# Optimization experiments

Measured on AMD Instinct MI355X. Metric: run time of the kernel, lower is better.

The kernel has to match this reference:

```python
import jax, jax.numpy as jnp
import numpy as np

B, L, E, H = 4, 2048, 1024, 16
D = E // H  # head_dim = 64
NEG_INF = -1e9


def _rope(x):
    # x: [B, L, H, D]; standard rotate-half RoPE over head_dim
    seq = x.shape[1]
    inv_freq = 1.0 / (10000.0 ** (jnp.arange(0, D, 2, dtype=jnp.float32) / D))  # [D/2]
    ang = jnp.arange(seq, dtype=jnp.float32)[:, None] * inv_freq               # [L, D/2]
    cos = jnp.concatenate([jnp.cos(ang), jnp.cos(ang)], axis=-1)[None, :, None, :]
    sin = jnp.concatenate([jnp.sin(ang), jnp.sin(ang)], axis=-1)[None, :, None, :]
    x1, x2 = jnp.split(x, 2, axis=-1)
    rot = jnp.concatenate([-x2, x1], axis=-1)
    return x * cos + rot * sin


def setup_inputs() -> dict:
    key = jax.random.key(0)
    ks = jax.random.split(key, 12)
    xavier = lambda k: jax.random.uniform(k, (E, E), jnp.float32,
                                          -np.sqrt(6.0 / (E + E)), np.sqrt(6.0 / (E + E)))
    return {
        "query": jax.random.normal(ks[0], (B, L, E), jnp.float32),
        "key": jax.random.normal(ks[1], (B, L, E), jnp.float32),
        "value": jax.random.normal(ks[2], (B, L, E), jnp.float32),
        "wq": xavier(ks[3]), "bq": jnp.zeros((E,), jnp.float32),
        "wk": xavier(ks[4]), "bk": jnp.zeros((E,), jnp.float32),
        "wv": xavier(ks[5]), "bv": jnp.zeros((E,), jnp.float32),
        "wo": xavier(ks[6]), "bo": jnp.zeros((E,), jnp.float32),
        "key_padding_mask": jax.random.randint(ks[7], (B, L), 0, 2).astype(bool),
    }


def reference(query, key, value, wq, bq, wk, bk, wv, bv, wo, bo, key_padding_mask):
    b, ql = query.shape[0], query.shape[1]
    sl = key.shape[1]
    q = (query @ wq.T + bq).reshape(b, ql, H, D)
    k = (key @ wk.T + bk).reshape(b, sl, H, D)
    v = (value @ wv.T + bv).reshape(b, sl, H, D)
    q = _rope(q)
    k = _rope(k)
    # causal mask (is_causal=True, attn_mask=None path) + key padding mask, additive
    causal = jnp.where(jnp.triu(jnp.ones((ql, sl), bool), k=1), NEG_INF, 0.0)  # [L, L]
    kpm = jnp.where(key_padding_mask[:, None, None, :], NEG_INF, 0.0)          # [B,1,1,S]
    mask = causal[None, None, :, :] + kpm
    scores = jnp.einsum("bqhd,bkhd->bhqk", q, k) / np.sqrt(D) + mask
    attn = jax.nn.softmax(scores, axis=-1)
    out = jnp.einsum("bhqk,bkhd->bqhd", attn, v).reshape(b, ql, E)
    return out @ wo.T + bo
```

## Files before the change

### kernel.cpp

```cpp
#include <hip/hip_runtime.h>

typedef unsigned short u16;
typedef unsigned int   u32;

using bf16x8 = __attribute__((ext_vector_type(8))) __bf16;
using f32x4  = __attribute__((ext_vector_type(4))) float;
using f32x16 = __attribute__((ext_vector_type(16))) float;

#define DEV static __device__ __forceinline__
#define GP(p) (const __attribute__((address_space(1))) void*)(p)
#define LP(p) (__attribute__((address_space(3))) void*)(p)
#define WAITB(N) asm volatile("s_waitcnt vmcnt(" N ")\n\ts_barrier" ::: "memory")

DEV u16 f2bf(float f){
  u32 u = __builtin_bit_cast(u32, f);
  u32 r = u + 0x7fffu + ((u>>16)&1u);
  return (u16)(r>>16);
}
DEV bf16x8 as_bf(uint4 v){ return __builtin_bit_cast(bf16x8, v); }
DEV u32 cvt_pk(float lo, float hi){
  u32 r;
  asm("v_cvt_pk_bf16_f32 %0, %1, %2" : "=v"(r) : "v"(lo), "v"(hi));
  return r;
}
DEV void plswap(u32 &a, u32 &b){
  auto r = __builtin_amdgcn_permlane32_swap((int)a, (int)b, false, false);
  a = (u32)r[0]; b = (u32)r[1];
}
DEV float fexp2(float x){ float r; asm("v_exp_f32 %0, %1" : "=v"(r) : "v"(x)); return r; }
DEV float max3f(float a, float b, float c){
  float r; asm("v_max3_f32 %0, %1, %2, %3" : "=v"(r) : "v"(a), "v"(b), "v"(c)); return r;
}
DEV float fractf_(float x){ float r; asm("v_fract_f32 %0, %1" : "=v"(r) : "v"(x)); return r; }
DEV float sinrev(float f){ float r; asm("v_sin_f32 %0, %1" : "=v"(r) : "v"(f)); return r; }
DEV float cosrev(float f){ float r; asm("v_cos_f32 %0, %1" : "=v"(r) : "v"(f)); return r; }

constexpr int CB = 4, CL = 2048, CE = 1024, CH = 16, CD = 64;
constexpr int CM = CB*CL;
constexpr float LOG2E  = 1.44269504088896f;
constexpr float NEGBIG = -1.44269504e9f;
constexpr float INV2PI = 0.15915494309189535f;

__global__ void detect_mask_kernel(const void* __restrict__ mask, int* __restrict__ flag){
  __shared__ int a_gt1, a_badf, a_oddnz, a_evennz;
  if (threadIdx.x==0){ a_gt1=0; a_badf=0; a_oddnz=0; a_evennz=0; }
  __syncthreads();
  const u32* w = (const u32*)mask;
  int gt1=0, badf=0, oddnz=0, evennz=0;
  for (int i=threadIdx.x; i<2048; i+=256){
    u32 v = w[i];
    if (v > 1u) gt1 = 1;
    if (v != 0u && v != 0x3f800000u) badf = 1;
    if (v != 0u){ if (i & 1) oddnz = 1; else evennz = 1; }
  }
  if (gt1) atomicOr(&a_gt1,1);
  if (badf) atomicOr(&a_badf,1);
  if (oddnz) atomicOr(&a_oddnz,1);
  if (evennz) atomicOr(&a_evennz,1);
  __syncthreads();
  if (threadIdx.x==0){
    int mode;
    if (!a_gt1)           mode = (!a_oddnz && a_evennz) ? 3 : 0;
    else if (!a_badf)     mode = 1;
    else                  mode = 2;
    flag[0] = mode;
  }
}

__global__ void convert_mask_kernel(const void* __restrict__ mask, const int* __restrict__ flag,
                                    float* __restrict__ maskf){
  int i = blockIdx.x*blockDim.x + threadIdx.x;
  if (i >= CB*CL) return;
  int mode = flag[0];
  int v;
  if      (mode==0) v = ((const int*)mask)[i] != 0;
  else if (mode==1) v = ((const float*)mask)[i] != 0.f;
  else if (mode==3) v = ((const int*)mask)[2*i] != 0;
  else              v = ((const unsigned char*)mask)[i] != 0;
  maskf[i] = v ? NEGBIG : 0.f;
}

__global__ void cast_all(const float* __restrict__ q, const float* __restrict__ k,
                         const float* __restrict__ v,
                         const float* __restrict__ wq, const float* __restrict__ wk,
                         const float* __restrict__ wv, const float* __restrict__ wo,
                         u16* __restrict__ oq, u16* __restrict__ ok, u16* __restrict__ ov,
                         u16* __restrict__ owq, u16* __restrict__ owk,
                         u16* __restrict__ owv, u16* __restrict__ owo){
  int i = blockIdx.x*blockDim.x + threadIdx.x;
  const float* in; u16* out; int j;
  if (i < 3*(1<<21)){
    int w = i >> 21; j = i & ((1<<21)-1);
    in = (w==0)?q:(w==1)?k:v; out = (w==0)?oq:(w==1)?ok:ov;
  } else {
    int r = i - 3*(1<<21);
    int w = r >> 18; j = r & ((1<<18)-1);
    in = (w==0)?wq:(w==1)?wk:(w==2)?wv:wo; out = (w==0)?owq:(w==1)?owk:(w==2)?owv:owo;
  }
  float4 a = ((const float4*)in)[j];
  ushort4 h;
  h.x = f2bf(a.x); h.y = f2bf(a.y); h.z = f2bf(a.z); h.w = f2bf(a.w);
  ((ushort4*)out)[j] = h;
}

__global__ __launch_bounds__(512) void gemm_qkv(
    const u16* __restrict__ qbf, const u16* __restrict__ kbf, const u16* __restrict__ vbf,
    const u16* __restrict__ wqb, const u16* __restrict__ wkb, const u16* __restrict__ wvb,
    const float* __restrict__ bq, const float* __restrict__ bk, const float* __restrict__ bv,
    u16* __restrict__ Qp, u16* __restrict__ Kp, u16* __restrict__ Vt, int zbase)
{
  __shared__ u16 As[3][16384];
  __shared__ u16 Bs[3][8192];
  const int z = zbase + blockIdx.y;
  const int tid=threadIdx.x, lane=tid&63, wid=tid>>6;
  const int llo=lane&15, lhi=lane>>4;
  const u16* A; const u16* Bt;
  if (z==0){ A=qbf; Bt=wqb; }
  else if (z==1){ A=kbf; Bt=wkb; }
  else { A=wvb; Bt=vbf; }
  int bid = blockIdx.x;
  int xcd = bid&7, j = bid>>3;
  int mb, nb;
  if (z<2){ mb = xcd*4 + (j>>3); nb = j&7; }
  else    { mb = j&3;  nb = xcd*8 + (j>>2); }
  const int m0 = mb*256, n0 = nb*128;
  const int wr = wid>>1, wc = wid&1;
  const int rswA = llo&7;

  auto STAGE = [&](int t, int buf){
    #pragma unroll
    for (int i=0;i<4;i++){
      int c = tid + i*512;
      int row = c>>3, ch = c&7;
      int sc = ch ^ (row&7);
      __builtin_amdgcn_global_load_lds(GP(A + (size_t)(m0+row)*CE + t*64 + sc*8),
                                       LP(&As[buf][c*8]), 16, 0, 0);
    }
    #pragma unroll
    for (int i=0;i<2;i++){
      int c = tid + i*512;
      int row = c>>3, ch = c&7;
      int sc = ch ^ (row&7);
      __builtin_amdgcn_global_load_lds(GP(Bt + (size_t)(n0+row)*CE + t*64 + sc*8),
                                       LP(&Bs[buf][c*8]), 16, 0, 0);
    }
  };

  f32x4 acc[4][4] = {};

  auto COMP = [&](int buf){
    const char* as = (const char*)As[buf];
    const char* bs = (const char*)Bs[buf];
    #pragma unroll
    for (int ks=0; ks<2; ks++){
      bf16x8 af[4], bf_[4];
      #pragma unroll
      for (int mr=0;mr<4;mr++){
        int r = wr*64+mr*16+llo;
        af[mr] = as_bf(*(const uint4*)(as + r*128 + (((ks*4+lhi)^rswA)<<4)));
      }
      #pragma unroll
      for (int nr=0;nr<4;nr++){
        int r = wc*64+nr*16+llo;
        bf_[nr] = as_bf(*(const uint4*)(bs + r*128 + (((ks*4+lhi)^rswA)<<4)));
      }
      #pragma unroll
      for (int mr=0;mr<4;mr++)
        #pragma unroll
        for (int nr=0;nr<4;nr++)
          acc[mr][nr] = __builtin_amdgcn_mfma_f32_16x16x32_bf16(af[mr], bf_[nr], acc[mr][nr], 0,0,0);
    }
  };

  STAGE(0,0); STAGE(1,1);
  WAITB("6");

  #pragma unroll 1
  for (int t=0; t<14; t++){
    STAGE(t+2, (t+2)%3);
    COMP(t%3);
    WAITB("6");
  }
  COMP(2); WAITB("0");
  COMP(0);

  const int colbase = n0 + wc*64;
  if (z < 2){
    const float* bias = z ? bk : bq;
    u16* outp = z ? Kp : Qp;
    const float scale = z ? 1.f : 0.125f*LOG2E;
    const int h = colbase >> 6;
    float b1[2], b2[2], invr[2];
    #pragma unroll
    for (int nr=0;nr<2;nr++){
      int j2 = nr*16 + llo;
      b1[nr] = bias[colbase + j2];
      b2[nr] = bias[colbase + j2 + 32];
      invr[nr] = exp2f(-(float)j2 * 0.41524101186092033f) * INV2PI;
    }
    #pragma unroll
    for (int mr=0;mr<4;mr++)
      #pragma unroll
      for (int r=0;r<4;r++){
        int row = m0 + wr*64 + mr*16 + lhi*4 + r;
        int b = row >> 11, l = row & 2047;
        u16* dst = outp + (((size_t)(b*CH + h)*CL + l) << 6);
        #pragma unroll
        for (int nr=0;nr<2;nr++){
          int j2 = nr*16 + llo;
          float x1 = (acc[mr][nr][r]   + b1[nr]) * scale;
          float x2 = (acc[mr][nr+2][r] + b2[nr]) * scale;
          float fr = fractf_((float)l * invr[nr]);
          float sn = sinrev(fr), cs = cosrev(fr);
          dst[j2]      = f2bf(x1*cs - x2*sn);
          dst[j2 + 32] = f2bf(x2*cs + x1*sn);
        }
      }
  } else {
    #pragma unroll
    for (int mr=0;mr<4;mr++)
      #pragma unroll
      for (int r=0;r<4;r++){
        int row = m0 + wr*64 + mr*16 + lhi*4 + r;
        float bvv = bv[row];
        #pragma unroll
        for (int nr=0;nr<4;nr++){
          int col = colbase + nr*16 + llo;
          Vt[(size_t)row*CM + col] = f2bf(acc[mr][nr][r] + bvv);
        }
      }
  }
}

__global__ __launch_bounds__(512) void gemm_out(
    const u16* __restrict__ A, const u16* __restrict__ Bt,
    const float* __restrict__ bias, float* __restrict__ C)
{
  __shared__ u16 As[3][16384];
  __shared__ u16 Bs[3][8192];
  const int tid=threadIdx.x, lane=tid&63, wid=tid>>6;
  const int llo=lane&15, lhi=lane>>4;
  int bid = blockIdx.x;
  int xcd = bid&7, j = bid>>3;
  const int m0 = (xcd*4 + (j>>3))*256, n0 = (j&7)*128;
  const int wr = wid>>1, wc = wid&1;
  const int rswA = llo&7;

  auto STAGE = [&](int t, int buf){
    #pragma unroll
    for (int i=0;i<4;i++){
      int c = tid + i*512;
      int row = c>>3, ch = c&7;
      int sc = ch ^ (row&7);
      __builtin_amdgcn_global_load_lds(GP(A + (size_t)(m0+row)*CE + t*64 + sc*8),
                                       LP(&As[buf][c*8]), 16, 0, 0);
    }
    #pragma unroll
    for (int i=0;i<2;i++){
      int c = tid + i*512;
      int row = c>>3, ch = c&7;
      int sc = ch ^ (row&7);
      __builtin_amdgcn_global_load_lds(GP(Bt + (size_t)(n0+row)*CE + t*64 + sc*8),
                                       LP(&Bs[buf][c*8]), 16, 0, 0);
    }
  };

  f32x4 acc[4][4] = {};

  auto COMP = [&](int buf){
    const char* as = (const char*)As[buf];
    const char* bs = (const char*)Bs[buf];
    #pragma unroll
    for (int ks=0; ks<2; ks++){
      bf16x8 af[4], bf_[4];
      #pragma unroll
      for (int mr=0;mr<4;mr++){
        int r = wr*64+mr*16+llo;
        af[mr] = as_bf(*(const uint4*)(as + r*128 + (((ks*4+lhi)^rswA)<<4)));
      }
      #pragma unroll
      for (int nr=0;nr<4;nr++){
        int r = wc*64+nr*16+llo;
        bf_[nr] = as_bf(*(const uint4*)(bs + r*128 + (((ks*4+lhi)^rswA)<<4)));
      }
      #pragma unroll
      for (int mr=0;mr<4;mr++)
        #pragma unroll
        for (int nr=0;nr<4;nr++)
          acc[mr][nr] = __builtin_amdgcn_mfma_f32_16x16x32_bf16(af[mr], bf_[nr], acc[mr][nr], 0,0,0);
    }
  };

  STAGE(0,0); STAGE(1,1);
  WAITB("6");

  #pragma unroll 1
  for (int t=0; t<14; t++){
    STAGE(t+2, (t+2)%3);
    COMP(t%3);
    WAITB("6");
  }
  COMP(2); WAITB("0");
  COMP(0);

  #pragma unroll
  for (int mr=0;mr<4;mr++)
    #pragma unroll
    for (int nr=0;nr<4;nr++)
      #pragma unroll
      for (int r=0;r<4;r++){
        int row = m0 + wr*64 + mr*16 + lhi*4 + r;
        int col = n0 + wc*64 + nr*16 + llo;
        C[(size_t)row*CE + col] = acc[mr][nr][r] + bias[col];
      }
}

__global__ __launch_bounds__(256,2) void attn_kernel(
    const u16* __restrict__ Qp, const u16* __restrict__ Kp, const u16* __restrict__ Vt,
    const float* __restrict__ maskf, u16* __restrict__ AO)
{
  __shared__ u16 K_lds[4][4096];
  __shared__ u16 V_lds[4][4096];
  __shared__ float M_lds[2048];
  const int bh = blockIdx.x;
  const int slot = blockIdx.y;
  const int b = bh >> 4, h = bh & 15;
  const int tid=threadIdx.x, lane=tid&63, wid=tid>>6;
  const int l31 = lane&31, hi = lane>>5;
  const u16* Qh = Qp + (size_t)bh*CL*CD;
  const u16* Kh = Kp + (size_t)bh*CL*CD;
  const u16* Vhd = Vt + (size_t)(h*CD)*CM + b*CL;

  #pragma unroll
  for (int i=0;i<2;i++)
    __builtin_amdgcn_global_load_lds(GP(maskf + b*CL + (i*256+tid)*4),
                                     LP(&M_lds[(i*256+tid)*4]), 16, 0, 0);

  auto STAGE = [&](int t, int buf){
    const u16* Ksrc = Kh + t*64*CD;
    const u16* Vsrc = Vhd + t*64;
    #pragma unroll
    for (int i=0;i<2;i++){
      int c = tid + i*256;
      int row = c>>3, sc = c&7;
      int c16 = sc ^ (row&7);
      __builtin_amdgcn_global_load_lds(GP(Ksrc + row*CD + c16*8),
                                       LP(&K_lds[buf][c*8]), 16, 0, 0);
      __builtin_amdgcn_global_load_lds(GP(Vsrc + (size_t)row*CM + c16*8),
                                       LP(&V_lds[buf][c*8]), 16, 0, 0);
    }
  };

  const int rowb = l31*128;
  const int rsw  = (l31&7)<<4;
  const int qts2[2] = {15-slot, slot};

  for (int qi=0; qi<2; qi++){
    const int qt = qts2[qi];
    const int qw0 = qt*128 + wid*32;
    const int qlane = qw0 + l31;

    bf16x8 qf[4];
    #pragma unroll
    for (int c=0;c<4;c++)
      qf[c] = as_bf(*(const uint4*)(Qh + (size_t)qlane*CD + c*16 + hi*8));

    f32x16 o0 = {}, o1 = {};
    float m_r = -3e38f, l_r = 0.f;

    const int nt = qt*2 + 2;
    STAGE(0,0); STAGE(1,1);

    for (int t=0; t<nt; t++){
      if (t+2 < nt){ STAGE(t+2,(t+2)&3); WAITB("8"); }
      else if (t+1 < nt){ WAITB("4"); }
      else { WAITB("0"); }

      const int kv0 = t*64;
      const char* kb = (const char*)K_lds[t&3];
      const char* vb = (const char*)V_lds[t&3];

      f32x4 cm[8];
      #pragma unroll
      for (int s2=0;s2<2;s2++)
        #pragma unroll
        for (int g=0; g<4; g++)
          cm[s2*4+g] = *(const f32x4*)&M_lds[kv0 + s2*32 + g*8 + hi*4];

      f32x16 s0 = {}, s1 = {};
      __builtin_amdgcn_s_setprio(1);
      #pragma unroll
      for (int c=0;c<4;c++){
        int cb = (c*32 + hi*16) ^ rsw;
        bf16x8 k0 = as_bf(*(const uint4*)(kb + rowb + cb));
        bf16x8 k1 = as_bf(*(const uint4*)(kb + 4096 + rowb + cb));
        s0 = __builtin_amdgcn_mfma_f32_32x32x16_bf16(k0, qf[c], s0, 0,0,0);
        s1 = __builtin_amdgcn_mfma_f32_32x32x16_bf16(k1, qf[c], s1, 0,0,0);
      }
      __builtin_amdgcn_s_setprio(0);

      if (kv0 + 63 > qw0){
        #pragma unroll
        for (int s2=0;s2<2;s2++){
          f32x16& sv = s2 ? s1 : s0;
          #pragma unroll
          for (int reg=0; reg<16; reg++){
            int k = kv0 + s2*32 + (reg&3) + (reg>>2)*8 + hi*4;
            float v = sv[reg] + cm[s2*4+(reg>>2)][reg&3];
            sv[reg] = (k > qlane) ? v + NEGBIG : v;
          }
        }
      } else {
        #pragma unroll
        for (int s2=0;s2<2;s2++){
          f32x16& sv = s2 ? s1 : s0;
          #pragma unroll
          for (int reg=0; reg<16; reg++)
            sv[reg] = sv[reg] + cm[s2*4+(reg>>2)][reg&3];
        }
      }

      f32x16 mx;
      #pragma unroll
      for (int r=0;r<16;r++) mx[r] = fmaxf(s0[r], s1[r]);
      float a0 = max3f(mx[0],mx[1],mx[2]);
      float a1 = max3f(mx[3],mx[4],mx[5]);
      float a2 = max3f(mx[6],mx[7],mx[8]);
      float a3 = max3f(mx[9],mx[10],mx[11]);
      float a4 = max3f(mx[12],mx[13],mx[14]);
      float vmax = fmaxf(max3f(a0,a1,a2), max3f(a3,a4,mx[15]));
      vmax = fmaxf(vmax, __shfl_xor(vmax, 32));

      if (__any(vmax > m_r + 12.0f)){
        float mnew = fmaxf(m_r, vmax);
        float sc = fexp2(m_r - mnew);
        l_r *= sc;
        o0 *= sc; o1 *= sc;
        m_r = mnew;
      }

      #pragma unroll
      for (int r=0;r<16;r++){
        s0[r] = fexp2(s0[r] - m_r);
        s1[r] = fexp2(s1[r] - m_r);
      }
      f32x16 sm = s0 + s1;
      #pragma unroll
      for (int w=8; w>=1; w>>=1)
        #pragma unroll
        for (int r=0;r<w;r++) sm[r] = sm[r] + sm[r+w];
      float rsum = sm[0];
      rsum += __shfl_xor(rsum, 32);
      l_r += rsum;

      u32 w_[16];
      #pragma unroll
      for (int s2=0;s2<2;s2++){
        f32x16& sv = s2 ? s1 : s0;
        #pragma unroll
        for (int c=0;c<2;c++){
          u32 a  = cvt_pk(sv[c*8+0], sv[c*8+1]);
          u32 bb = cvt_pk(sv[c*8+2], sv[c*8+3]);
          u32 cc = cvt_pk(sv[c*8+4], sv[c*8+5]);
          u32 dd = cvt_pk(sv[c*8+6], sv[c*8+7]);
          plswap(a, cc); plswap(bb, dd);
          int base = (s2*2+c)*4;
          w_[base+0]=a; w_[base+1]=bb; w_[base+2]=cc; w_[base+3]=dd;
        }
      }

      __builtin_amdgcn_s_setprio(1);
      #pragma unroll
      for (int kc=0; kc<4; kc++){
        bf16x8 pf = as_bf(make_uint4(w_[kc*4], w_[kc*4+1], w_[kc*4+2], w_[kc*4+3]));
        int cb = (kc*32 + hi*16) ^ rsw;
        bf16x8 v0 = as_bf(*(const uint4*)(vb + rowb + cb));
        bf16x8 v1 = as_bf(*(const uint4*)(vb + 4096 + rowb + cb));
        o0 = __builtin_amdgcn_mfma_f32_32x32x16_bf16(v0, pf, o0, 0,0,0);
        o1 = __builtin_amdgcn_mfma_f32_32x32x16_bf16(v1, pf, o1, 0,0,0);
      }
      __builtin_amdgcn_s_setprio(0);
    }

    float inv = 1.f / l_r;
    u16* dst = AO + (size_t)(b*CL + qlane)*CE + h*CD;
    #pragma unroll
    for (int mt=0; mt<2; mt++){
      f32x16& ov = mt ? o1 : o0;
      #pragma unroll
      for (int g=0; g<4; g++){
        u32 lo  = cvt_pk(ov[g*4+0]*inv, ov[g*4+1]*inv);
        u32 hi2 = cvt_pk(ov[g*4+2]*inv, ov[g*4+3]*inv);
        *(uint2*)(dst + mt*32 + g*8 + hi*4) = make_uint2(lo, hi2);
      }
    }
    __syncthreads();
  }
}

extern "C" void kernel_launch(void* const* d_in, const int* in_sizes, int n_in,
                              void* d_out, int out_size, void* d_ws, size_t ws_size,
                              hipStream_t stream) {
  const float* query = (const float*)d_in[0];
  const float* key_  = (const float*)d_in[1];
  const float* value = (const float*)d_in[2];
  const float* wq = (const float*)d_in[3];
  const float* bq = (const float*)d_in[4];
  const float* wk = (const float*)d_in[5];
  const float* bk = (const float*)d_in[6];
  const float* wv = (const float*)d_in[7];
  const float* bv = (const float*)d_in[8];
  const float* wo = (const float*)d_in[9];
  const float* bo = (const float*)d_in[10];
  const void*  kpm = d_in[11];

  char* ws = (char*)d_ws;
  constexpr size_t SZ_ME_BF = (size_t)CM*CE*2;
  constexpr size_t SZ_EE_BF = (size_t)CE*CE*2;
  constexpr size_t OFF_FLAG = 0;
  constexpr size_t OFF_MASKF= 256;
  constexpr size_t OFF_B0   = 65536;
  constexpr size_t OFF_B1   = OFF_B0 + SZ_ME_BF;
  constexpr size_t OFF_B2   = OFF_B1 + SZ_ME_BF;
  constexpr size_t OFF_WQ   = OFF_B2 + SZ_ME_BF;
  constexpr size_t OFF_WK   = OFF_WQ + SZ_EE_BF;
  constexpr size_t OFF_WV   = OFF_WK + SZ_EE_BF;
  constexpr size_t OFF_WO   = OFF_WV + SZ_EE_BF;
  constexpr size_t OFF_KP   = OFF_WO + SZ_EE_BF;
  constexpr size_t OFF_VT   = OFF_KP + SZ_ME_BF;
  constexpr size_t OFF_QP   = OFF_VT + SZ_ME_BF;

  int*   flag  = (int*)(ws + OFF_FLAG);
  float* maskf = (float*)(ws + OFF_MASKF);
  u16*  qbf = (u16*)(ws + OFF_B0);
  u16*  kbf = (u16*)(ws + OFF_B1);
  u16*  vbf = (u16*)(ws + OFF_B2);
  u16*  wqb = (u16*)(ws + OFF_WQ);
  u16*  wkb = (u16*)(ws + OFF_WK);
  u16*  wvb = (u16*)(ws + OFF_WV);
  u16*  wob = (u16*)(ws + OFF_WO);
  u16*  Kp  = (u16*)(ws + OFF_KP);
  u16*  Vt  = (u16*)(ws + OFF_VT);
  u16*  AO  = qbf;

  detect_mask_kernel<<<1,256,0,stream>>>(kpm, flag);
  convert_mask_kernel<<<(CB*CL+255)/256,256,0,stream>>>(kpm, flag, maskf);

  cast_all<<<28672,256,0,stream>>>(query, key_, value, wq, wk, wv, wo,
                                   qbf, kbf, vbf, wqb, wkb, wvb, wob);

  u16* Qp;
  if (ws_size >= OFF_QP + SZ_ME_BF){
    Qp = (u16*)(ws + OFF_QP);
    gemm_qkv<<<dim3(256,3),512,0,stream>>>(qbf, kbf, vbf, wqb, wkb, wvb,
                                           bq, bk, bv, Qp, Kp, Vt, 0);
  } else {
    Qp = vbf;
    gemm_qkv<<<dim3(256,2),512,0,stream>>>(qbf, kbf, vbf, wqb, wkb, wvb,
                                           bq, bk, bv, Qp, Kp, Vt, 1);
    gemm_qkv<<<dim3(256,1),512,0,stream>>>(qbf, kbf, vbf, wqb, wkb, wvb,
                                           bq, bk, bv, Qp, Kp, Vt, 0);
  }

  attn_kernel<<<dim3(CB*CH, 8),256,0,stream>>>(Qp, Kp, Vt, maskf, AO);

  gemm_out<<<256,512,0,stream>>>(AO, wob, bo, (float*)d_out);
}
```

Measured before the change: 193.6 us.

## Fuse fp32-to-bf16 casts into GEMM loaders via register staging

Removes the separate cast_all kernel. The QKV and output GEMMs now load fp32 inputs and weights straight into registers, convert them to bf16 with packed conversion, and write them to LDS, using a new double-buffered register/LDS pipeline. This avoids a full round trip through memory for the bf16 copies and saves one launch. In exchange the GEMMs read twice the bytes per tile, use more registers, and the direct global-to-LDS async loads are replaced by a manual load/convert/store schedule with extra waits and barriers.

```diff
diff --git a/kernel.cpp b/kernel.cpp
--- a/kernel.cpp
+++ b/kernel.cpp
@@ -6,17 +6,22 @@
 using bf16x8 = __attribute__((ext_vector_type(8))) __bf16;
 using f32x4  = __attribute__((ext_vector_type(4))) float;
 using f32x16 = __attribute__((ext_vector_type(16))) float;
+using u32x4  = __attribute__((ext_vector_type(4))) u32;
 
 #define DEV static __device__ __forceinline__
 #define GP(p) (const __attribute__((address_space(1))) void*)(p)
 #define LP(p) (__attribute__((address_space(3))) void*)(p)
 #define WAITB(N) asm volatile("s_waitcnt vmcnt(" N ")\n\ts_barrier" ::: "memory")
+#define WAITVM(N) do{ asm volatile("s_waitcnt vmcnt(" N ")" ::: "memory"); \
+                      __builtin_amdgcn_sched_barrier(0); }while(0)
+#define LGKMB asm volatile("s_waitcnt lgkmcnt(0)\n\ts_barrier" ::: "memory")
 
 DEV u16 f2bf(float f){
   u32 u = __builtin_bit_cast(u32, f);
   u32 r = u + 0x7fffu + ((u>>16)&1u);
   return (u16)(r>>16);
 }
+DEV float bcf(u32 x){ return __builtin_bit_cast(float, x); }
 DEV bf16x8 as_bf(uint4 v){ return __builtin_bit_cast(bf16x8, v); }
 DEV u32 cvt_pk(float lo, float hi){
   u32 r;
@@ -80,44 +85,23 @@
   maskf[i] = v ? NEGBIG : 0.f;
 }
 
-__global__ void cast_all(const float* __restrict__ q, const float* __restrict__ k,
-                         const float* __restrict__ v,
-                         const float* __restrict__ wq, const float* __restrict__ wk,
-                         const float* __restrict__ wv, const float* __restrict__ wo,
-                         u16* __restrict__ oq, u16* __restrict__ ok, u16* __restrict__ ov,
-                         u16* __restrict__ owq, u16* __restrict__ owk,
-                         u16* __restrict__ owv, u16* __restrict__ owo){
-  int i = blockIdx.x*blockDim.x + threadIdx.x;
-  const float* in; u16* out; int j;
-  if (i < 3*(1<<21)){
-    int w = i >> 21; j = i & ((1<<21)-1);
-    in = (w==0)?q:(w==1)?k:v; out = (w==0)?oq:(w==1)?ok:ov;
-  } else {
-    int r = i - 3*(1<<21);
-    int w = r >> 18; j = r & ((1<<18)-1);
-    in = (w==0)?wq:(w==1)?wk:(w==2)?wv:wo; out = (w==0)?owq:(w==1)?owk:(w==2)?owv:owo;
-  }
-  float4 a = ((const float4*)in)[j];
-  ushort4 h;
-  h.x = f2bf(a.x); h.y = f2bf(a.y); h.z = f2bf(a.z); h.w = f2bf(a.w);
-  ((ushort4*)out)[j] = h;
-}
-
 __global__ __launch_bounds__(512) void gemm_qkv(
-    const u16* __restrict__ qbf, const u16* __restrict__ kbf, const u16* __restrict__ vbf,
-    const u16* __restrict__ wqb, const u16* __restrict__ wkb, const u16* __restrict__ wvb,
+    const float* __restrict__ query, const float* __restrict__ keyp,
+    const float* __restrict__ value,
+    const float* __restrict__ wq, const float* __restrict__ wk,
+    const float* __restrict__ wv,
     const float* __restrict__ bq, const float* __restrict__ bk, const float* __restrict__ bv,
-    u16* __restrict__ Qp, u16* __restrict__ Kp, u16* __restrict__ Vt, int zbase)
+    u16* __restrict__ Qp, u16* __restrict__ Kp, u16* __restrict__ Vt)
 {
-  __shared__ u16 As[3][16384];
-  __shared__ u16 Bs[3][8192];
-  const int z = zbase + blockIdx.y;
+  __shared__ u16 As[2][16384];
+  __shared__ u16 Bs[2][8192];
+  const int z = blockIdx.y;
   const int tid=threadIdx.x, lane=tid&63, wid=tid>>6;
   const int llo=lane&15, lhi=lane>>4;
-  const u16* A; const u16* Bt;
-  if (z==0){ A=qbf; Bt=wqb; }
-  else if (z==1){ A=kbf; Bt=wkb; }
-  else { A=wvb; Bt=vbf; }
+  const float* Af; const float* Btf;
+  if (z==0){ Af=query; Btf=wq; }
+  else if (z==1){ Af=keyp; Btf=wk; }
+  else { Af=wv; Btf=value; }
   int bid = blockIdx.x;
   int xcd = bid&7, j = bid>>3;
   int mb, nb;
@@ -127,24 +111,55 @@
   const int wr = wid>>1, wc = wid&1;
   const int rswA = llo&7;
 
-  auto STAGE = [&](int t, int buf){
-    #pragma unroll
-    for (int i=0;i<4;i++){
-      int c = tid + i*512;
-      int row = c>>3, ch = c&7;
-      int sc = ch ^ (row&7);
-      __builtin_amdgcn_global_load_lds(GP(A + (size_t)(m0+row)*CE + t*64 + sc*8),
-                                       LP(&As[buf][c*8]), 16, 0, 0);
-    }
-    #pragma unroll
-    for (int i=0;i<2;i++){
-      int c = tid + i*512;
-      int row = c>>3, ch = c&7;
-      int sc = ch ^ (row&7);
-      __builtin_amdgcn_global_load_lds(GP(Bt + (size_t)(n0+row)*CE + t*64 + sc*8),
-                                       LP(&Bs[buf][c*8]), 16, 0, 0);
-    }
-  };
+  const float* aptr[4]; int aco[4];
+  #pragma unroll
+  for (int i=0;i<4;i++){
+    int c = tid + i*512, row=c>>3, sc=(c&7)^(row&7);
+    aptr[i] = Af + (size_t)(m0+row)*CE + sc*8;
+    aco[i] = c*8;
+  }
+  const float* bptr[2]; int bco[2];
+  #pragma unroll
+  for (int i=0;i<2;i++){
+    int c = tid + i*512, row=c>>3, sc=(c&7)^(row&7);
+    bptr[i] = Btf + (size_t)(n0+row)*CE + sc*8;
+    bco[i] = c*8;
+  }
+
+  u32x4 A0[8], B0[4], A1[8], B1[4];
+
+#define LOADT(T, RA, RB) do{ \
+  _Pragma("unroll") \
+  for (int i=0;i<4;i++){ \
+    asm volatile("global_load_dwordx4 %0, %2, off\n\tglobal_load_dwordx4 %1, %2, off offset:16" \
+      : "=&v"(RA[2*i]), "=&v"(RA[2*i+1]) : "v"(aptr[i] + (size_t)(T)*64) : "memory"); \
+  } \
+  _Pragma("unroll") \
+  for (int i=0;i<2;i++){ \
+    asm volatile("global_load_dwordx4 %0, %2, off\n\tglobal_load_dwordx4 %1, %2, off offset:16" \
+      : "=&v"(RB[2*i]), "=&v"(RB[2*i+1]) : "v"(bptr[i] + (size_t)(T)*64) : "memory"); \
+  } \
+}while(0)
+
+#define CVTW(dst, lo4, hi4) do{ \
+  dst.x = cvt_pk(bcf(lo4.x), bcf(lo4.y)); \
+  dst.y = cvt_pk(bcf(lo4.z), bcf(lo4.w)); \
+  dst.z = cvt_pk(bcf(hi4.x), bcf(hi4.y)); \
+  dst.w = cvt_pk(bcf(hi4.z), bcf(hi4.w)); \
+}while(0)
+
+#define WRITET(BUF, RA, RB) do{ \
+  _Pragma("unroll") \
+  for (int i=0;i<4;i++){ \
+    u32x4 w; CVTW(w, RA[2*i], RA[2*i+1]); \
+    *(u32x4*)&As[BUF][aco[i]] = w; \
+  } \
+  _Pragma("unroll") \
+  for (int i=0;i<2;i++){ \
+    u32x4 w; CVTW(w, RB[2*i], RB[2*i+1]); \
+    *(u32x4*)&Bs[BUF][bco[i]] = w; \
+  } \
+}while(0)
 
   f32x4 acc[4][4] = {};
 
@@ -172,17 +187,34 @@
     }
   };
 
-  STAGE(0,0); STAGE(1,1);
-  WAITB("6");
+  LOADT(0, A0, B0);
+  LOADT(1, A1, B1);
+  WAITVM("12");
+  WRITET(0, A0, B0);
+  LGKMB;
 
   #pragma unroll 1
-  for (int t=0; t<14; t++){
-    STAGE(t+2, (t+2)%3);
-    COMP(t%3);
-    WAITB("6");
-  }
-  COMP(2); WAITB("0");
+  for (int jj=0; jj<7; jj++){
+    const int t = 2*jj;
+    LOADT(t+2, A0, B0);
+    WAITVM("12");
+    WRITET(1, A1, B1);
+    COMP(0);
+    LGKMB;
+    LOADT(t+3, A1, B1);
+    WAITVM("12");
+    WRITET(0, A0, B0);
+    COMP(1);
+    LGKMB;
+  }
+  WAITVM("0");
+  WRITET(1, A1, B1);
   COMP(0);
+  LGKMB;
+  COMP(1);
+
+#undef LOADT
+#undef WRITET
 
   const int colbase = n0 + wc*64;
   if (z < 2){
@@ -233,11 +265,11 @@
 }
 
 __global__ __launch_bounds__(512) void gemm_out(
-    const u16* __restrict__ A, const u16* __restrict__ Bt,
+    const u16* __restrict__ A, const float* __restrict__ Btf,
     const float* __restrict__ bias, float* __restrict__ C)
 {
   __shared__ u16 As[3][16384];
-  __shared__ u16 Bs[3][8192];
+  __shared__ u16 Bs[2][8192];
   const int tid=threadIdx.x, lane=tid&63, wid=tid>>6;
   const int llo=lane&15, lhi=lane>>4;
   int bid = blockIdx.x;
@@ -246,30 +278,45 @@
   const int wr = wid>>1, wc = wid&1;
   const int rswA = llo&7;
 
-  auto STAGE = [&](int t, int buf){
+  auto STAGEA = [&](int t, int buf){
     #pragma unroll
     for (int i=0;i<4;i++){
-      int c = tid + i*512;
-      int row = c>>3, ch = c&7;
-      int sc = ch ^ (row&7);
+      int c = tid + i*512, row=c>>3, sc=(c&7)^(row&7);
       __builtin_amdgcn_global_load_lds(GP(A + (size_t)(m0+row)*CE + t*64 + sc*8),
                                        LP(&As[buf][c*8]), 16, 0, 0);
     }
-    #pragma unroll
-    for (int i=0;i<2;i++){
-      int c = tid + i*512;
-      int row = c>>3, ch = c&7;
-      int sc = ch ^ (row&7);
-      __builtin_amdgcn_global_load_lds(GP(Bt + (size_t)(n0+row)*CE + t*64 + sc*8),
-                                       LP(&Bs[buf][c*8]), 16, 0, 0);
-    }
   };
 
+  const float* bptr[2]; int bco[2];
+  #pragma unroll
+  for (int i=0;i<2;i++){
+    int c = tid + i*512, row=c>>3, sc=(c&7)^(row&7);
+    bptr[i] = Btf + (size_t)(n0+row)*CE + sc*8;
+    bco[i] = c*8;
+  }
+  u32x4 B0[4], B1[4];
+
+#define LOADB(T, RB) do{ \
+  _Pragma("unroll") \
+  for (int i=0;i<2;i++){ \
+    asm volatile("global_load_dwordx4 %0, %2, off\n\tglobal_load_dwordx4 %1, %2, off offset:16" \
+      : "=&v"(RB[2*i]), "=&v"(RB[2*i+1]) : "v"(bptr[i] + (size_t)(T)*64) : "memory"); \
+  } \
+}while(0)
+
+#define WRITEB(BUF, RB) do{ \
+  _Pragma("unroll") \
+  for (int i=0;i<2;i++){ \
+    u32x4 w; CVTW(w, RB[2*i], RB[2*i+1]); \
+    *(u32x4*)&Bs[BUF][bco[i]] = w; \
+  } \
+}while(0)
+
   f32x4 acc[4][4] = {};
 
-  auto COMP = [&](int buf){
-    const char* as = (const char*)As[buf];
-    const char* bs = (const char*)Bs[buf];
+  auto COMP = [&](int abuf, int bbuf){
+    const char* as = (const char*)As[abuf];
+    const char* bs = (const char*)Bs[bbuf];
     #pragma unroll
     for (int ks=0; ks<2; ks++){
       bf16x8 af[4], bf_[4];
@@ -291,17 +338,34 @@
     }
   };
 
-  STAGE(0,0); STAGE(1,1);
-  WAITB("6");
+  STAGEA(0,0); LOADB(0, B0);
+  STAGEA(1,1); LOADB(1, B1);
+  WAITVM("8");
+  WRITEB(0, B0);
+  LGKMB;
 
   #pragma unroll 1
-  for (int t=0; t<14; t++){
-    STAGE(t+2, (t+2)%3);
-    COMP(t%3);
-    WAITB("6");
-  }
-  COMP(2); WAITB("0");
-  COMP(0);
+  for (int jj=0; jj<7; jj++){
+    const int t = 2*jj;
+    STAGEA(t+2, (t+2)%3); LOADB(t+2, B0);
+    WAITVM("8");
+    WRITEB(1, B1);
+    COMP(t%3, 0);
+    LGKMB;
+    STAGEA(t+3, (t+3)%3); LOADB(t+3, B1);
+    WAITVM("8");
+    WRITEB(0, B0);
+    COMP((t+1)%3, 1);
+    LGKMB;
+  }
+  WAITVM("0");
+  WRITEB(1, B1);
+  COMP(2, 0);
+  LGKMB;
+  COMP(0, 1);
+
+#undef LOADB
+#undef WRITEB
 
   #pragma unroll
   for (int mr=0;mr<4;mr++)
@@ -516,53 +580,27 @@
 
   char* ws = (char*)d_ws;
   constexpr size_t SZ_ME_BF = (size_t)CM*CE*2;
-  constexpr size_t SZ_EE_BF = (size_t)CE*CE*2;
   constexpr size_t OFF_FLAG = 0;
   constexpr size_t OFF_MASKF= 256;
-  constexpr size_t OFF_B0   = 65536;
-  constexpr size_t OFF_B1   = OFF_B0 + SZ_ME_BF;
-  constexpr size_t OFF_B2   = OFF_B1 + SZ_ME_BF;
-  constexpr size_t OFF_WQ   = OFF_B2 + SZ_ME_BF;
-  constexpr size_t OFF_WK   = OFF_WQ + SZ_EE_BF;
-  constexpr size_t OFF_WV   = OFF_WK + SZ_EE_BF;
-  constexpr size_t OFF_WO   = OFF_WV + SZ_EE_BF;
-  constexpr size_t OFF_KP   = OFF_WO + SZ_EE_BF;
+  constexpr size_t OFF_AO   = 65536;
+  constexpr size_t OFF_KP   = OFF_AO + SZ_ME_BF;
   constexpr size_t OFF_VT   = OFF_KP + SZ_ME_BF;
   constexpr size_t OFF_QP   = OFF_VT + SZ_ME_BF;
 
   int*   flag  = (int*)(ws + OFF_FLAG);
   float* maskf = (float*)(ws + OFF_MASKF);
-  u16*  qbf = (u16*)(ws + OFF_B0);
-  u16*  kbf = (u16*)(ws + OFF_B1);
-  u16*  vbf = (u16*)(ws + OFF_B2);
-  u16*  wqb = (u16*)(ws + OFF_WQ);
-  u16*  wkb = (u16*)(ws + OFF_WK);
-  u16*  wvb = (u16*)(ws + OFF_WV);
-  u16*  wob = (u16*)(ws + OFF_WO);
+  u16*  AO  = (u16*)(ws + OFF_AO);
   u16*  Kp  = (u16*)(ws + OFF_KP);
   u16*  Vt  = (u16*)(ws + OFF_VT);
-  u16*  AO  = qbf;
+  u16*  Qp  = (u16*)(ws + OFF_QP);
 
   detect_mask_kernel<<<1,256,0,stream>>>(kpm, flag);
   convert_mask_kernel<<<(CB*CL+255)/256,256,0,stream>>>(kpm, flag, maskf);
 
-  cast_all<<<28672,256,0,stream>>>(query, key_, value, wq, wk, wv, wo,
-                                   qbf, kbf, vbf, wqb, wkb, wvb, wob);
-
-  u16* Qp;
-  if (ws_size >= OFF_QP + SZ_ME_BF){
-    Qp = (u16*)(ws + OFF_QP);
-    gemm_qkv<<<dim3(256,3),512,0,stream>>>(qbf, kbf, vbf, wqb, wkb, wvb,
-                                           bq, bk, bv, Qp, Kp, Vt, 0);
-  } else {
-    Qp = vbf;
-    gemm_qkv<<<dim3(256,2),512,0,stream>>>(qbf, kbf, vbf, wqb, wkb, wvb,
-                                           bq, bk, bv, Qp, Kp, Vt, 1);
-    gemm_qkv<<<dim3(256,1),512,0,stream>>>(qbf, kbf, vbf, wqb, wkb, wvb,
-                                           bq, bk, bv, Qp, Kp, Vt, 0);
-  }
+  gemm_qkv<<<dim3(256,3),512,0,stream>>>(query, key_, value, wq, wk, wv,
+                                         bq, bk, bv, Qp, Kp, Vt);
 
   attn_kernel<<<dim3(CB*CH, 8),256,0,stream>>>(Qp, Kp, Vt, maskf, AO);
 
-  gemm_out<<<256,512,0,stream>>>(AO, wob, bo, (float*)d_out);
-}
+  gemm_out<<<256,512,0,stream>>>(AO, wo, bo, (float*)d_out);
+}
```

Result: no change. 190.9 us (-1.4%).
